# Optimization experiments

Measured on AMD Instinct MI355X. Metric: run time of the kernel, lower is better.

## Reference

```python
import jax, jax.numpy as jnp
import numpy as np

DEPTH = 3  # weights are SHARED across depth (same module object repeated in ModuleList)


def prelu(x, a):
    # nn.PReLU() with a single shared slope parameter
    return jnp.where(x >= 0, x, a * x)


def conv1x1(x, w, b):
    # x: (N,C,H,W), w: (O,C), b: (O,)
    return jnp.einsum('nchw,oc->nohw', x, w) + b[None, :, None, None]


def conv3x3(x, w, b):
    # w: (O,I,3,3), padding=1 stride=1 -> SAME
    y = jax.lax.conv_general_dilated(x, w, (1, 1), 'SAME',
                                     dimension_numbers=('NCHW', 'OIHW', 'NCHW'))
    return y + b[None, :, None, None]


def _unit(x, w1, b1, a1, w2, b2, a2, w3, b3, a3, wc, bc):
    # NonLocalAttention
    e1 = prelu(conv1x1(x, w1, b1), a1)   # (N,C,H,W)
    e2 = prelu(conv1x1(x, w2, b2), a2)   # (N,C,H,W)
    asm = prelu(conv1x1(x, w3, b3), a3)  # (N,C,H,W)
    N, C, H, W = e1.shape
    q = e1.reshape(N, C, H * W).transpose(0, 2, 1)     # (N,HW,C)
    k = e2.reshape(N, C, H * W)                        # (N,C,HW)
    score = jax.nn.softmax(jnp.matmul(q, k), axis=2)   # (N,HW,HW)
    v = asm.reshape(N, C, H * W).transpose(0, 2, 1)    # (N,HW,C)
    att = jnp.matmul(score, v).transpose(0, 2, 1).reshape(N, C, H, W)
    # Conv2d(channel, channel, 3, 1, 1) + exact GELU
    return jax.nn.gelu(conv3x3(att, wc, bc), approximate=False)


def setup_inputs() -> dict:
    key = jax.random.key(0)
    ks = jax.random.split(key, 8)
    C = 128
    x = jax.random.normal(ks[0], (1, C, 96, 96), dtype=jnp.float32)
    s = 0.05
    inp = {
        'x': x,
        'w1': jax.random.normal(ks[1], (C, C), jnp.float32) * s,
        'b1': jnp.zeros((C,), jnp.float32),
        'a1': jnp.float32(0.25),
        'w2': jax.random.normal(ks[2], (C, C), jnp.float32) * s,
        'b2': jnp.zeros((C,), jnp.float32),
        'a2': jnp.float32(0.25),
        'w3': jax.random.normal(ks[3], (C, C), jnp.float32) * s,
        'b3': jnp.zeros((C,), jnp.float32),
        'a3': jnp.float32(0.25),
        'wc': jax.random.normal(ks[4], (C, C, 3, 3), jnp.float32) * s,
        'bc': jnp.zeros((C,), jnp.float32),
    }
    return inp


def reference(x, w1, b1, a1, w2, b2, a2, w3, b3, a3, wc, bc):
    res = x
    for _ in range(DEPTH):  # same (shared) weights each iteration, per original module
        res = _unit(res, w1, b1, a1, w2, b2, a2, w3, b3, a3, wc, bc)
    return x + res
```

## Files before the change

### kernel.cpp

```cpp
#include <hip/hip_runtime.h>

#define HWPX 9216
#define NCH  128

typedef float  f32x4  __attribute__((ext_vector_type(4)));
typedef __bf16 bf16x8 __attribute__((ext_vector_type(8)));

#define SWZ16(row) ((((row) & 7) ^ (((row) >> 3) << 1)) << 4)

__global__ __launch_bounds__(256) void prep_kernel(
    const float* __restrict__ w1, const float* __restrict__ w2,
    const float* __restrict__ w3, const float* __restrict__ wc,
    const float* __restrict__ x,
    __bf16* __restrict__ Wb, __bf16* __restrict__ wck,
    __bf16* __restrict__ Xb) {
  int tid = blockIdx.x * 256 + threadIdx.x;
  int nt  = gridDim.x * 256;
  for (int idx = tid; idx < 3 * 16384; idx += nt) {
    int j = idx >> 14;
    const float* w = (j == 0) ? w1 : (j == 1 ? w2 : w3);
    Wb[idx] = (__bf16)w[idx & 16383];
  }
  for (int idx = tid; idx < 147456; idx += nt) {
    int k = idx % 9;
    int rest = idx / 9;
    int c = rest & 127, o = rest >> 7;
    wck[(k * 128 + o) * 128 + c] = (__bf16)wc[idx];
  }
  for (int idx = tid; idx < 128 * HWPX; idx += nt) {
    int c = idx / HWPX, p = idx - c * HWPX;
    Xb[p * 128 + c] = (__bf16)x[idx];
  }
}

__global__ __launch_bounds__(256) void conv1x1_qkv(
    const __bf16* __restrict__ Xb, const __bf16* __restrict__ Wb,
    const float* __restrict__ b1, const float* __restrict__ b2,
    const float* __restrict__ b3, const float* __restrict__ a1,
    const float* __restrict__ a2, const float* __restrict__ a3,
    __bf16* __restrict__ Q, __bf16* __restrict__ K, __bf16* __restrict__ Vt) {
  const int tid = threadIdx.x, lane = tid & 63, w = tid >> 6;
  const int l16 = lane & 15, hi = lane >> 4;
  const int p0 = blockIdx.x * 64;

  bf16x8 af[4][4];
#pragma unroll
  for (int pxt = 0; pxt < 4; ++pxt)
#pragma unroll
    for (int kc = 0; kc < 4; ++kc)
      af[pxt][kc] = *(const bf16x8*)&Xb[(p0 + pxt * 16 + l16) * 128 + kc * 32 + hi * 8];

  const float s1 = a1[0], s2 = a2[0], s3 = a3[0];

#pragma unroll
  for (int ot = 0; ot < 6; ++ot) {
    const int obase = w * 96 + ot * 16;
    const int j = obase >> 7;
    const int oo = (obase & 127) + l16;
    bf16x8 bfg[4];
#pragma unroll
    for (int kc = 0; kc < 4; ++kc)
      bfg[kc] = *(const bf16x8*)&Wb[(obase + l16) * 128 + kc * 32 + hi * 8];
    f32x4 acc[4];
#pragma unroll
    for (int pxt = 0; pxt < 4; ++pxt) acc[pxt] = (f32x4){0.f, 0.f, 0.f, 0.f};
#pragma unroll
    for (int kc = 0; kc < 4; ++kc)
#pragma unroll
      for (int pxt = 0; pxt < 4; ++pxt)
        acc[pxt] = __builtin_amdgcn_mfma_f32_16x16x32_bf16(af[pxt][kc], bfg[kc], acc[pxt], 0, 0, 0);

    const float* bp = (j == 0) ? b1 : (j == 1 ? b2 : b3);
    const float bias = bp[oo];
    const float sl = (j == 0) ? s1 : (j == 1 ? s2 : s3);
#pragma unroll
    for (int pxt = 0; pxt < 4; ++pxt)
#pragma unroll
      for (int r = 0; r < 4; ++r) {
        float v = acc[pxt][r] + bias;
        v = (v >= 0.f) ? v : sl * v;
        int px = p0 + pxt * 16 + hi * 4 + r;
        if (j == 0)      Q[px * 128 + oo] = (__bf16)v;
        else if (j == 1) K[px * 128 + oo] = (__bf16)v;
        else             Vt[oo * HWPX + px] = (__bf16)v;
      }
  }
}

__global__ __launch_bounds__(512) void flash_attn(
    const __bf16* __restrict__ Q, const __bf16* __restrict__ Kb,
    const __bf16* __restrict__ Vt, float* __restrict__ Opart,
    float* __restrict__ mOut, float* __restrict__ lOut, int nt) {
  __shared__ __align__(16) unsigned char smem[81920];
  const int tid  = threadIdx.x;
  const int lane = tid & 63;
  const int w    = tid >> 6;
  const int l16  = lane & 15;
  const int hi   = lane >> 4;
  const int qb   = blockIdx.x * 128;
  const int kt0  = blockIdx.y * nt;

  const __bf16* gsrc[4];
  unsigned loff[4];
  long gstep;
  if (w < 4) {
    gstep = 8192;
#pragma unroll
    for (int j = 0; j < 4; ++j) {
      int seg = w * 4 + j;
      int row = seg * 4 + (lane >> 4);
      int ch  = lane & 15;
      gsrc[j] = Kb + (size_t)(kt0 * 64 + row) * 128 + (ch ^ (row & 7)) * 8;
      loff[j] = seg * 1024;
    }
  } else {
    gstep = 64;
#pragma unroll
    for (int j = 0; j < 4; ++j) {
      int seg = (w - 4) * 4 + j;
      int d  = seg * 8 + (lane >> 3);
      int ch = lane & 7;
      gsrc[j] = Vt + (size_t)d * HWPX + kt0 * 64 + (ch ^ (d & 7)) * 8;
      loff[j] = 16384 + seg * 1024;
    }
  }

#define STAGE(BUF) do {                                                        \
  _Pragma("unroll")                                                            \
  for (int j = 0; j < 4; ++j) {                                                \
    __builtin_amdgcn_global_load_lds(                                          \
        (const __attribute__((address_space(1))) unsigned int*)gsrc[j],        \
        (__attribute__((address_space(3))) unsigned int*)(smem + (BUF) * 32768 \
                                                          + loff[j]),          \
        16, 0, 0);                                                             \
    gsrc[j] += gstep;                                                          \
  } } while (0)

  bf16x8 qf[4];
  const int qrow = qb + w * 16 + l16;
#pragma unroll
  for (int dc = 0; dc < 4; ++dc)
    qf[dc] = *(const bf16x8*)&Q[qrow * 128 + dc * 32 + hi * 8];

  f32x4 oacc[8];
#pragma unroll
  for (int dc = 0; dc < 8; ++dc) oacc[dc] = (f32x4){0.f, 0.f, 0.f, 0.f};
  float m[4], l[4];
#pragma unroll
  for (int r = 0; r < 4; ++r) { m[r] = -INFINITY; l[r] = 0.f; }

  const unsigned pbase = 65536 + w * 2048;

  STAGE(0);
  __syncthreads();

  int cur = 0;
  for (int it = 0; it < nt; ++it) {
    if (it + 1 < nt) STAGE(cur ^ 1);

    const unsigned kb0 = cur * 32768;
    f32x4 s[4];
#pragma unroll
    for (int g = 0; g < 4; ++g) {
      s[g] = (f32x4){0.f, 0.f, 0.f, 0.f};
      int row = g * 16 + l16;
#pragma unroll
      for (int dc = 0; dc < 4; ++dc) {
        bf16x8 kf = *(const bf16x8*)&smem[kb0 + row * 256 +
                        ((dc * 64 + hi * 16) ^ ((row & 7) << 4))];
        s[g] = __builtin_amdgcn_mfma_f32_16x16x32_bf16(qf[dc], kf, s[g], 0, 0, 0);
      }
    }

    float mx[4];
#pragma unroll
    for (int r = 0; r < 4; ++r) {
      mx[r] = fmaxf(fmaxf(s[0][r], s[1][r]), fmaxf(s[2][r], s[3][r]));
      mx[r] = fmaxf(mx[r], __shfl_xor(mx[r], 1));
      mx[r] = fmaxf(mx[r], __shfl_xor(mx[r], 2));
      mx[r] = fmaxf(mx[r], __shfl_xor(mx[r], 4));
      mx[r] = fmaxf(mx[r], __shfl_xor(mx[r], 8));
    }
    float alpha[4], rs[4];
#pragma unroll
    for (int r = 0; r < 4; ++r) {
      float mn = fmaxf(m[r], mx[r]);
      alpha[r] = __expf(m[r] - mn);
      m[r] = mn;
      rs[r] = 0.f;
    }
#pragma unroll
    for (int g = 0; g < 4; ++g)
#pragma unroll
      for (int r = 0; r < 4; ++r) {
        float p = __expf(s[g][r] - m[r]);
        s[g][r] = p;
        rs[r] += p;
      }
#pragma unroll
    for (int r = 0; r < 4; ++r) {
      rs[r] += __shfl_xor(rs[r], 1);
      rs[r] += __shfl_xor(rs[r], 2);
      rs[r] += __shfl_xor(rs[r], 4);
      rs[r] += __shfl_xor(rs[r], 8);
      l[r] = l[r] * alpha[r] + rs[r];
    }
#pragma unroll
    for (int dc = 0; dc < 8; ++dc)
#pragma unroll
      for (int r = 0; r < 4; ++r) oacc[dc][r] *= alpha[r];

#pragma unroll
    for (int g = 0; g < 4; ++g)
#pragma unroll
      for (int r = 0; r < 4; ++r) {
        int row = hi * 4 + r;
        *(__bf16*)&smem[pbase + row * 128 +
                        ((g * 32 + l16 * 2) ^ SWZ16(row))] = (__bf16)s[g][r];
      }
    bf16x8 pa[2];
#pragma unroll
    for (int kc = 0; kc < 2; ++kc)
      pa[kc] = *(const bf16x8*)&smem[pbase + l16 * 128 +
                   ((kc * 64 + hi * 16) ^ SWZ16(l16))];
#pragma unroll
    for (int dc = 0; dc < 8; ++dc) {
#pragma unroll
      for (int kc = 0; kc < 2; ++kc) {
        int row = dc * 16 + l16;
        bf16x8 vf = *(const bf16x8*)&smem[kb0 + 16384 + row * 128 +
                        ((kc * 64 + hi * 16) ^ ((row & 7) << 4))];
        oacc[dc] = __builtin_amdgcn_mfma_f32_16x16x32_bf16(pa[kc], vf, oacc[dc], 0, 0, 0);
      }
    }
    __syncthreads();
    cur ^= 1;
  }
#undef STAGE

  const int sbase = blockIdx.y * HWPX;
#pragma unroll
  for (int dc = 0; dc < 8; ++dc)
#pragma unroll
    for (int r = 0; r < 4; ++r) {
      int q = qb + w * 16 + hi * 4 + r;
      Opart[(size_t)(sbase + q) * 128 + dc * 16 + l16] = oacc[dc][r];
    }
  if (l16 == 0) {
#pragma unroll
    for (int r = 0; r < 4; ++r) {
      int q = qb + w * 16 + hi * 4 + r;
      mOut[sbase + q] = m[r];
      lOut[sbase + q] = l[r];
    }
  }
}

__global__ __launch_bounds__(256) void flash_combine(
    const float* __restrict__ Opart, const float* __restrict__ mArr,
    const float* __restrict__ lArr, float* __restrict__ att, int ksplit) {
  int idx = blockIdx.x * 256 + threadIdx.x;
  int q = idx >> 5, d4 = idx & 31;
  float M = -INFINITY;
  for (int i = 0; i < ksplit; ++i) M = fmaxf(M, mArr[i * HWPX + q]);
  float denom = 0.f;
  f32x4 acc = (f32x4){0.f, 0.f, 0.f, 0.f};
  for (int i = 0; i < ksplit; ++i) {
    float wi = __expf(mArr[i * HWPX + q] - M);
    denom += lArr[i * HWPX + q] * wi;
    f32x4 v = *(const f32x4*)&Opart[((size_t)i * HWPX + q) * 128 + d4 * 4];
#pragma unroll
    for (int e = 0; e < 4; ++e) acc[e] += wi * v[e];
  }
  float inv = 1.f / denom;
  f32x4 r;
#pragma unroll
  for (int e = 0; e < 4; ++e) r[e] = acc[e] * inv;
  *(f32x4*)&att[(size_t)q * 128 + d4 * 4] = r;
}

__global__ __launch_bounds__(256) void conv3x3_gelu(
    const float* __restrict__ att, const __bf16* __restrict__ wck,
    const float* __restrict__ bc, const float* __restrict__ resid,
    float* __restrict__ out, __bf16* __restrict__ xbo) {
  __shared__ __align__(16) unsigned char smem[38400];
  const int tid = threadIdx.x;
  const int y   = blockIdx.x >> 1;
  const int x0  = (blockIdx.x & 1) * 48;
  const int lane = tid & 63, w = tid >> 6;
  const int l16 = lane & 15, hi = lane >> 4;

  for (int id = tid; id < 2400; id += 256) {
    int px = id >> 4, ch = id & 15;
    int hy = px / 50, hx = px - hy * 50;
    int gy = y + hy - 1, gx = x0 + hx - 1;
    bf16x8 v;
    if (gy >= 0 && gy < 96 && gx >= 0 && gx < 96) {
      const float* src = &att[(gy * 96 + gx) * 128 + ch * 8];
      f32x4 aa = *(const f32x4*)src;
      f32x4 bb = *(const f32x4*)(src + 4);
#pragma unroll
      for (int e = 0; e < 4; ++e) { v[e] = (__bf16)aa[e]; v[4 + e] = (__bf16)bb[e]; }
    } else {
#pragma unroll
      for (int e = 0; e < 8; ++e) v[e] = (__bf16)0.f;
    }
    *(bf16x8*)&smem[px * 256 + ((ch * 16) ^ ((px & 7) << 4))] = v;
  }
  __syncthreads();

  f32x4 acc[2][3];
#pragma unroll
  for (int ot = 0; ot < 2; ++ot) {
    int obase = w * 32 + ot * 16 + hi * 4;
#pragma unroll
    for (int pt = 0; pt < 3; ++pt)
#pragma unroll
      for (int r = 0; r < 4; ++r) acc[ot][pt][r] = bc[obase + r];
  }

  for (int tap = 0; tap < 9; ++tap) {
    int dy = tap / 3, dx = tap - dy * 3;
#pragma unroll
    for (int cc = 0; cc < 4; ++cc) {
      bf16x8 af[2];
#pragma unroll
      for (int ot = 0; ot < 2; ++ot)
        af[ot] = *(const bf16x8*)&wck[(tap * 128 + w * 32 + ot * 16 + l16) * 128 +
                                      cc * 32 + hi * 8];
#pragma unroll
      for (int pt = 0; pt < 3; ++pt) {
        int px = dy * 50 + pt * 16 + l16 + dx;
        bf16x8 bf = *(const bf16x8*)&smem[px * 256 +
                        ((cc * 64 + hi * 16) ^ ((px & 7) << 4))];
#pragma unroll
        for (int ot = 0; ot < 2; ++ot)
          acc[ot][pt] = __builtin_amdgcn_mfma_f32_16x16x32_bf16(af[ot], bf, acc[ot][pt], 0, 0, 0);
      }
    }
  }

  float ge[2][3][4];
#pragma unroll
  for (int ot = 0; ot < 2; ++ot)
#pragma unroll
    for (int pt = 0; pt < 3; ++pt)
#pragma unroll
      for (int r = 0; r < 4; ++r) {
        float v = acc[ot][pt][r];
        ge[ot][pt][r] = 0.5f * v * (1.f + erff(v * 0.70710678118654752f));
      }

  if (xbo) {
    __syncthreads();
#pragma unroll
    for (int ot = 0; ot < 2; ++ot)
#pragma unroll
      for (int pt = 0; pt < 3; ++pt)
#pragma unroll
        for (int r = 0; r < 4; ++r) {
          int o  = w * 32 + ot * 16 + hi * 4 + r;
          int pl = pt * 16 + l16;
          *(__bf16*)&smem[pl * 256 + ((o * 2) ^ ((pl & 7) << 4))] =
              (__bf16)ge[ot][pt][r];
        }
    __syncthreads();
    for (int id = tid; id < 768; id += 256) {
      int pl = id >> 4, ch = id & 15;
      bf16x8 v = *(const bf16x8*)&smem[pl * 256 + ((ch * 16) ^ ((pl & 7) << 4))];
      *(bf16x8*)&xbo[(size_t)(y * 96 + x0 + pl) * 128 + ch * 8] = v;
    }
  } else {
#pragma unroll
    for (int ot = 0; ot < 2; ++ot)
#pragma unroll
      for (int pt = 0; pt < 3; ++pt)
#pragma unroll
        for (int r = 0; r < 4; ++r) {
          int o  = w * 32 + ot * 16 + hi * 4 + r;
          int px = y * 96 + x0 + pt * 16 + l16;
          out[o * HWPX + px] = ge[ot][pt][r] + resid[o * HWPX + px];
        }
  }
}

extern "C" void kernel_launch(void* const* d_in, const int* in_sizes, int n_in,
                              void* d_out, int out_size, void* d_ws, size_t ws_size,
                              hipStream_t stream) {
  const float* x  = (const float*)d_in[0];
  const float* w1 = (const float*)d_in[1];
  const float* b1 = (const float*)d_in[2];
  const float* a1 = (const float*)d_in[3];
  const float* w2 = (const float*)d_in[4];
  const float* b2 = (const float*)d_in[5];
  const float* a2 = (const float*)d_in[6];
  const float* w3 = (const float*)d_in[7];
  const float* b3 = (const float*)d_in[8];
  const float* a3 = (const float*)d_in[9];
  const float* wc = (const float*)d_in[10];
  const float* bc = (const float*)d_in[11];
  float* out = (float*)d_out;

  char* ws = (char*)d_ws;
  float*  att = (float*)(ws + 0);
  __bf16* Qb  = (__bf16*)(ws + 4718592);
  __bf16* Kb  = (__bf16*)(ws + 7077888);
  __bf16* Vt  = (__bf16*)(ws + 9437184);
  __bf16* Xb  = (__bf16*)(ws + 11796480);
  __bf16* Wb  = (__bf16*)(ws + 14155776);
  __bf16* wck = (__bf16*)(ws + 14254080);
  const size_t base_end = 14548992;

  int ksplit = 1;
  if (ws_size >= base_end + 8ull * (4718592 + 2 * 36864)) ksplit = 8;
  else if (ws_size >= base_end + 4ull * (4718592 + 2 * 36864)) ksplit = 4;
  else if (ws_size >= base_end + 2ull * (4718592 + 2 * 36864)) ksplit = 2;
  float* Opart = (float*)(ws + base_end);
  float* mArr  = (float*)(ws + base_end + (size_t)ksplit * 4718592);
  float* lArr  = (float*)(ws + base_end + (size_t)ksplit * (4718592 + 36864));

  prep_kernel<<<576, 256, 0, stream>>>(w1, w2, w3, wc, x, Wb, wck, Xb);

  for (int u = 0; u < 3; ++u) {
    conv1x1_qkv<<<144, 256, 0, stream>>>(Xb, Wb, b1, b2, b3, a1, a2, a3,
                                         Qb, Kb, Vt);
    flash_attn<<<dim3(72, ksplit), 512, 0, stream>>>(
        Qb, Kb, Vt, Opart, mArr, lArr, 144 / ksplit);
    flash_combine<<<1152, 256, 0, stream>>>(Opart, mArr, lArr, att, ksplit);
    conv3x3_gelu<<<192, 256, 0, stream>>>(att, wck, bc,
                                          (u == 2) ? x : nullptr,
                                          (u == 2) ? out : nullptr,
                                          (u < 2) ? Xb : nullptr);
  }
}
```

Measured before the change: 542.2 us.

## Split qkv and conv3x3 grids, add lazy softmax rescale, DPP reductions, setprio

The 1x1 QKV conv now spreads its six output tiles across a second grid dimension, and the 3x3 conv uses 32-pixel tiles with 288 blocks, so more blocks run at once. In flash attention, the row max and sum reductions use DPP instead of shuffles, and MFMA sections are wrapped in s_setprio. Blocks are reordered so the k-splits of one query tile run next to each other. The online softmax skips the rescale unless the max grows by more than 8, which lowers per-tile exp and multiply work but lets unnormalised values grow up to e^8 before correction.

```diff
diff --git a/kernel.cpp b/kernel.cpp
--- a/kernel.cpp
+++ b/kernel.cpp
@@ -7,6 +7,20 @@
 typedef __bf16 bf16x8 __attribute__((ext_vector_type(8)));
 
 #define SWZ16(row) ((((row) & 7) ^ (((row) >> 3) << 1)) << 4)
+
+#define DPP_RED(v, OP)                                                         \
+  do {                                                                         \
+    v = OP(v, __int_as_float(__builtin_amdgcn_update_dpp(                      \
+               0, __float_as_int(v), 0xB1, 0xF, 0xF, true)));                  \
+    v = OP(v, __int_as_float(__builtin_amdgcn_update_dpp(                      \
+               0, __float_as_int(v), 0x4E, 0xF, 0xF, true)));                  \
+    v = OP(v, __int_as_float(__builtin_amdgcn_update_dpp(                      \
+               0, __float_as_int(v), 0x124, 0xF, 0xF, true)));                 \
+    v = OP(v, __int_as_float(__builtin_amdgcn_update_dpp(                      \
+               0, __float_as_int(v), 0x128, 0xF, 0xF, true)));                 \
+  } while (0)
+__device__ __forceinline__ float op_max(float a, float b) { return fmaxf(a, b); }
+__device__ __forceinline__ float op_add(float a, float b) { return a + b; }
 
 __global__ __launch_bounds__(256) void prep_kernel(
     const float* __restrict__ w1, const float* __restrict__ w2,
@@ -42,6 +56,7 @@
   const int tid = threadIdx.x, lane = tid & 63, w = tid >> 6;
   const int l16 = lane & 15, hi = lane >> 4;
   const int p0 = blockIdx.x * 64;
+  const int z  = blockIdx.y;
 
   bf16x8 af[4][4];
 #pragma unroll
@@ -50,41 +65,37 @@
     for (int kc = 0; kc < 4; ++kc)
       af[pxt][kc] = *(const bf16x8*)&Xb[(p0 + pxt * 16 + l16) * 128 + kc * 32 + hi * 8];
 
-  const float s1 = a1[0], s2 = a2[0], s3 = a3[0];
-
-#pragma unroll
-  for (int ot = 0; ot < 6; ++ot) {
-    const int obase = w * 96 + ot * 16;
-    const int j = obase >> 7;
-    const int oo = (obase & 127) + l16;
-    bf16x8 bfg[4];
-#pragma unroll
-    for (int kc = 0; kc < 4; ++kc)
-      bfg[kc] = *(const bf16x8*)&Wb[(obase + l16) * 128 + kc * 32 + hi * 8];
-    f32x4 acc[4];
-#pragma unroll
-    for (int pxt = 0; pxt < 4; ++pxt) acc[pxt] = (f32x4){0.f, 0.f, 0.f, 0.f};
-#pragma unroll
-    for (int kc = 0; kc < 4; ++kc)
-#pragma unroll
-      for (int pxt = 0; pxt < 4; ++pxt)
-        acc[pxt] = __builtin_amdgcn_mfma_f32_16x16x32_bf16(af[pxt][kc], bfg[kc], acc[pxt], 0, 0, 0);
-
-    const float* bp = (j == 0) ? b1 : (j == 1 ? b2 : b3);
-    const float bias = bp[oo];
-    const float sl = (j == 0) ? s1 : (j == 1 ? s2 : s3);
+  const int obase = w * 96 + z * 16;
+  const int j = obase >> 7;
+  const int oo = (obase & 127) + l16;
+  bf16x8 bfg[4];
+#pragma unroll
+  for (int kc = 0; kc < 4; ++kc)
+    bfg[kc] = *(const bf16x8*)&Wb[(obase + l16) * 128 + kc * 32 + hi * 8];
+  f32x4 acc[4];
+#pragma unroll
+  for (int pxt = 0; pxt < 4; ++pxt) acc[pxt] = (f32x4){0.f, 0.f, 0.f, 0.f};
+#pragma unroll
+  for (int kc = 0; kc < 4; ++kc)
 #pragma unroll
     for (int pxt = 0; pxt < 4; ++pxt)
-#pragma unroll
-      for (int r = 0; r < 4; ++r) {
-        float v = acc[pxt][r] + bias;
-        v = (v >= 0.f) ? v : sl * v;
-        int px = p0 + pxt * 16 + hi * 4 + r;
-        if (j == 0)      Q[px * 128 + oo] = (__bf16)v;
-        else if (j == 1) K[px * 128 + oo] = (__bf16)v;
-        else             Vt[oo * HWPX + px] = (__bf16)v;
-      }
-  }
+      acc[pxt] = __builtin_amdgcn_mfma_f32_16x16x32_bf16(af[pxt][kc], bfg[kc], acc[pxt], 0, 0, 0);
+
+  const float* bp = (j == 0) ? b1 : (j == 1 ? b2 : b3);
+  const float bias = bp[oo];
+  const float* ap = (j == 0) ? a1 : (j == 1 ? a2 : a3);
+  const float sl = ap[0];
+#pragma unroll
+  for (int pxt = 0; pxt < 4; ++pxt)
+#pragma unroll
+    for (int r = 0; r < 4; ++r) {
+      float v = acc[pxt][r] + bias;
+      v = (v >= 0.f) ? v : sl * v;
+      int px = p0 + pxt * 16 + hi * 4 + r;
+      if (j == 0)      Q[px * 128 + oo] = (__bf16)v;
+      else if (j == 1) K[px * 128 + oo] = (__bf16)v;
+      else             Vt[oo * HWPX + px] = (__bf16)v;
+    }
 }
 
 __global__ __launch_bounds__(512) void flash_attn(
@@ -97,8 +108,11 @@
   const int w    = tid >> 6;
   const int l16  = lane & 15;
   const int hi   = lane >> 4;
-  const int qb   = blockIdx.x * 128;
-  const int kt0  = blockIdx.y * nt;
+  const int ord  = blockIdx.y * 72 + blockIdx.x;
+  const int nsp  = gridDim.y;
+  const int split = ord % nsp;
+  const int qb   = (ord / nsp) * 128;
+  const int kt0  = split * nt;
 
   const __bf16* gsrc[4];
   unsigned loff[4];
@@ -160,6 +174,7 @@
 
     const unsigned kb0 = cur * 32768;
     f32x4 s[4];
+    __builtin_amdgcn_s_setprio(1);
 #pragma unroll
     for (int g = 0; g < 4; ++g) {
       s[g] = (f32x4){0.f, 0.f, 0.f, 0.f};
@@ -171,24 +186,31 @@
         s[g] = __builtin_amdgcn_mfma_f32_16x16x32_bf16(qf[dc], kf, s[g], 0, 0, 0);
       }
     }
+    __builtin_amdgcn_s_setprio(0);
 
     float mx[4];
 #pragma unroll
     for (int r = 0; r < 4; ++r) {
       mx[r] = fmaxf(fmaxf(s[0][r], s[1][r]), fmaxf(s[2][r], s[3][r]));
-      mx[r] = fmaxf(mx[r], __shfl_xor(mx[r], 1));
-      mx[r] = fmaxf(mx[r], __shfl_xor(mx[r], 2));
-      mx[r] = fmaxf(mx[r], __shfl_xor(mx[r], 4));
-      mx[r] = fmaxf(mx[r], __shfl_xor(mx[r], 8));
-    }
-    float alpha[4], rs[4];
-#pragma unroll
-    for (int r = 0; r < 4; ++r) {
-      float mn = fmaxf(m[r], mx[r]);
-      alpha[r] = __expf(m[r] - mn);
-      m[r] = mn;
-      rs[r] = 0.f;
-    }
+      DPP_RED(mx[r], op_max);
+    }
+    bool need = false;
+#pragma unroll
+    for (int r = 0; r < 4; ++r) need = need || (mx[r] > m[r] + 8.f);
+    if (__any(need)) {
+#pragma unroll
+      for (int r = 0; r < 4; ++r) {
+        float mn = fmaxf(m[r], mx[r]);
+        float alpha = __expf(m[r] - mn);
+        m[r] = mn;
+        l[r] *= alpha;
+#pragma unroll
+        for (int dc = 0; dc < 8; ++dc) oacc[dc][r] *= alpha;
+      }
+    }
+    float rs[4];
+#pragma unroll
+    for (int r = 0; r < 4; ++r) rs[r] = 0.f;
 #pragma unroll
     for (int g = 0; g < 4; ++g)
 #pragma unroll
@@ -199,16 +221,9 @@
       }
 #pragma unroll
     for (int r = 0; r < 4; ++r) {
-      rs[r] += __shfl_xor(rs[r], 1);
-      rs[r] += __shfl_xor(rs[r], 2);
-      rs[r] += __shfl_xor(rs[r], 4);
-      rs[r] += __shfl_xor(rs[r], 8);
-      l[r] = l[r] * alpha[r] + rs[r];
-    }
-#pragma unroll
-    for (int dc = 0; dc < 8; ++dc)
-#pragma unroll
-      for (int r = 0; r < 4; ++r) oacc[dc][r] *= alpha[r];
+      DPP_RED(rs[r], op_add);
+      l[r] += rs[r];
+    }
 
 #pragma unroll
     for (int g = 0; g < 4; ++g)
@@ -223,6 +238,7 @@
     for (int kc = 0; kc < 2; ++kc)
       pa[kc] = *(const bf16x8*)&smem[pbase + l16 * 128 +
                    ((kc * 64 + hi * 16) ^ SWZ16(l16))];
+    __builtin_amdgcn_s_setprio(1);
 #pragma unroll
     for (int dc = 0; dc < 8; ++dc) {
 #pragma unroll
@@ -233,12 +249,13 @@
         oacc[dc] = __builtin_amdgcn_mfma_f32_16x16x32_bf16(pa[kc], vf, oacc[dc], 0, 0, 0);
       }
     }
+    __builtin_amdgcn_s_setprio(0);
     __syncthreads();
     cur ^= 1;
   }
 #undef STAGE
 
-  const int sbase = blockIdx.y * HWPX;
+  const int sbase = split * HWPX;
 #pragma unroll
   for (int dc = 0; dc < 8; ++dc)
 #pragma unroll
@@ -283,16 +300,16 @@
     const float* __restrict__ att, const __bf16* __restrict__ wck,
     const float* __restrict__ bc, const float* __restrict__ resid,
     float* __restrict__ out, __bf16* __restrict__ xbo) {
-  __shared__ __align__(16) unsigned char smem[38400];
+  __shared__ __align__(16) unsigned char smem[26112];
   const int tid = threadIdx.x;
-  const int y   = blockIdx.x >> 1;
-  const int x0  = (blockIdx.x & 1) * 48;
+  const int y   = blockIdx.x / 3;
+  const int x0  = (blockIdx.x % 3) * 32;
   const int lane = tid & 63, w = tid >> 6;
   const int l16 = lane & 15, hi = lane >> 4;
 
-  for (int id = tid; id < 2400; id += 256) {
+  for (int id = tid; id < 1632; id += 256) {
     int px = id >> 4, ch = id & 15;
-    int hy = px / 50, hx = px - hy * 50;
+    int hy = px / 34, hx = px - hy * 34;
     int gy = y + hy - 1, gx = x0 + hx - 1;
     bf16x8 v;
     if (gy >= 0 && gy < 96 && gx >= 0 && gx < 96) {
@@ -309,12 +326,12 @@
   }
   __syncthreads();
 
-  f32x4 acc[2][3];
+  f32x4 acc[2][2];
 #pragma unroll
   for (int ot = 0; ot < 2; ++ot) {
     int obase = w * 32 + ot * 16 + hi * 4;
 #pragma unroll
-    for (int pt = 0; pt < 3; ++pt)
+    for (int pt = 0; pt < 2; ++pt)
 #pragma unroll
       for (int r = 0; r < 4; ++r) acc[ot][pt][r] = bc[obase + r];
   }
@@ -329,8 +346,8 @@
         af[ot] = *(const bf16x8*)&wck[(tap * 128 + w * 32 + ot * 16 + l16) * 128 +
                                       cc * 32 + hi * 8];
 #pragma unroll
-      for (int pt = 0; pt < 3; ++pt) {
-        int px = dy * 50 + pt * 16 + l16 + dx;
+      for (int pt = 0; pt < 2; ++pt) {
+        int px = dy * 34 + pt * 16 + l16 + dx;
         bf16x8 bf = *(const bf16x8*)&smem[px * 256 +
                         ((cc * 64 + hi * 16) ^ ((px & 7) << 4))];
 #pragma unroll
@@ -340,11 +357,11 @@
     }
   }
 
-  float ge[2][3][4];
+  float ge[2][2][4];
 #pragma unroll
   for (int ot = 0; ot < 2; ++ot)
 #pragma unroll
-    for (int pt = 0; pt < 3; ++pt)
+    for (int pt = 0; pt < 2; ++pt)
 #pragma unroll
       for (int r = 0; r < 4; ++r) {
         float v = acc[ot][pt][r];
@@ -356,7 +373,7 @@
 #pragma unroll
     for (int ot = 0; ot < 2; ++ot)
 #pragma unroll
-      for (int pt = 0; pt < 3; ++pt)
+      for (int pt = 0; pt < 2; ++pt)
 #pragma unroll
         for (int r = 0; r < 4; ++r) {
           int o  = w * 32 + ot * 16 + hi * 4 + r;
@@ -365,7 +382,7 @@
               (__bf16)ge[ot][pt][r];
         }
     __syncthreads();
-    for (int id = tid; id < 768; id += 256) {
+    for (int id = tid; id < 512; id += 256) {
       int pl = id >> 4, ch = id & 15;
       bf16x8 v = *(const bf16x8*)&smem[pl * 256 + ((ch * 16) ^ ((pl & 7) << 4))];
       *(bf16x8*)&xbo[(size_t)(y * 96 + x0 + pl) * 128 + ch * 8] = v;
@@ -374,7 +391,7 @@
 #pragma unroll
     for (int ot = 0; ot < 2; ++ot)
 #pragma unroll
-      for (int pt = 0; pt < 3; ++pt)
+      for (int pt = 0; pt < 2; ++pt)
 #pragma unroll
         for (int r = 0; r < 4; ++r) {
           int o  = w * 32 + ot * 16 + hi * 4 + r;
@@ -422,12 +439,12 @@
   prep_kernel<<<576, 256, 0, stream>>>(w1, w2, w3, wc, x, Wb, wck, Xb);
 
   for (int u = 0; u < 3; ++u) {
-    conv1x1_qkv<<<144, 256, 0, stream>>>(Xb, Wb, b1, b2, b3, a1, a2, a3,
-                                         Qb, Kb, Vt);
+    conv1x1_qkv<<<dim3(144, 6), 256, 0, stream>>>(Xb, Wb, b1, b2, b3, a1, a2, a3,
+                                                  Qb, Kb, Vt);
     flash_attn<<<dim3(72, ksplit), 512, 0, stream>>>(
         Qb, Kb, Vt, Opart, mArr, lArr, 144 / ksplit);
     flash_combine<<<1152, 256, 0, stream>>>(Opart, mArr, lArr, att, ksplit);
-    conv3x3_gelu<<<192, 256, 0, stream>>>(att, wck, bc,
+    conv3x3_gelu<<<288, 256, 0, stream>>>(att, wck, bc,
                                           (u == 2) ? x : nullptr,
                                           (u == 2) ? out : nullptr,
                                           (u < 2) ? Xb : nullptr);
```

After: 476.0 us. -12.2%, faster.
